# Kernel tuning notes

Hardware: AMD Instinct MI355X
Metric: run time of the kernel (lower is better)

Reference implementation:

```python
import jax, jax.numpy as jnp
import numpy as np

B, C, H, NP, M = 32, 768, 12, 196, 64
D = C // H
GRID = 14  # sqrt(196)
NG = 1 + NP  # cls + patches = 197
EPS = 1e-5


def _ln(x, w, b):
    mu = x.mean(-1, keepdims=True)
    var = ((x - mu) ** 2).mean(-1, keepdims=True)
    return (x - mu) * jax.lax.rsqrt(var + EPS) * w + b


def setup_inputs() -> dict:
    key = jax.random.key(0)
    ks = jax.random.split(key, 14)
    std = 0.02
    return {
        "x": jax.random.normal(ks[0], (B, NG + M, C), dtype=jnp.float32),
        "ps": jax.random.uniform(ks[1], (B, M, 2), dtype=jnp.float32) * 224.0,
        "ns": jax.random.randint(ks[2], (B,), 1, M + 1, dtype=jnp.int32),
        "norm1_w": jnp.ones((C,), jnp.float32),
        "norm1_b": jnp.zeros((C,), jnp.float32),
        "qkv_w": jax.random.normal(ks[3], (3 * C, C), jnp.float32) * std,
        "proj_w": jax.random.normal(ks[4], (C, C), jnp.float32) * std,
        "proj_b": jnp.zeros((C,), jnp.float32),
        "norm2_w": jnp.ones((C,), jnp.float32),
        "norm2_b": jnp.zeros((C,), jnp.float32),
        "fc1_w": jax.random.normal(ks[5], (4 * C, C), jnp.float32) * std,
        "fc1_b": jnp.zeros((4 * C,), jnp.float32),
        "fc2_w": jax.random.normal(ks[6], (C, 4 * C), jnp.float32) * std,
        "fc2_b": jnp.zeros((C,), jnp.float32),
    }


def reference(x, ps, ns, norm1_w, norm1_b, qkv_w, proj_w, proj_b,
              norm2_w, norm2_b, fc1_w, fc1_b, fc2_w, fc2_b):
    Bn, Nt, Cd = x.shape  # Nt = 1 + 196 + M
    scale = D ** -0.5

    h = _ln(x, norm1_w, norm1_b)
    qkv = (h @ qkv_w.T).reshape(Bn, Nt, 3, H, D).transpose(2, 0, 3, 1, 4)  # [3,B,H,Nt,D]
    q, k, v = qkv[0], qkv[1], qkv[2]

    # ---- global attention over cls + patch tokens (first 197) ----
    attn = jnp.einsum('bhnd,bhmd->bhnm', q[:, :, :NG], k[:, :, :NG]) * scale
    attn = jax.nn.softmax(attn, axis=-1)
    xg = jnp.einsum('bhnm,bhmd->bhnd', attn, v[:, :, :NG])
    xg = xg.transpose(0, 2, 1, 3).reshape(Bn, NG, Cd)  # [B,197,C]

    # ---- keypoint bilinear-gather attention (get_single_filter_matrix) ----
    pos = ps / 16.0  # [B,M,2]; pos[...,1] -> row (dim 4), pos[...,0] -> col (dim 5)
    c0 = jnp.clip(jnp.floor(pos[..., 0]), 0, GRID - 1).astype(jnp.int32)
    c1 = jnp.clip(jnp.ceil(pos[..., 0]), 0, GRID - 1).astype(jnp.int32)
    r0 = jnp.clip(jnp.floor(pos[..., 1]), 0, GRID - 1).astype(jnp.int32)
    r1 = jnp.clip(jnp.ceil(pos[..., 1]), 0, GRID - 1).astype(jnp.int32)
    # neighbor order: top_left, top_right, bottom_left, bottom_right
    rows = jnp.stack([r0, r1, r0, r1], axis=-1)  # [B,M,4]
    cols = jnp.stack([c0, c0, c1, c1], axis=-1)
    flat = rows * GRID + cols  # [B,M,4] flat index into 196 patch tokens

    kp = k[:, :, 1:NG]  # [B,H,196,D]
    vp = v[:, :, 1:NG]
    idx = jnp.broadcast_to(flat.reshape(Bn, 1, M * 4, 1), (Bn, H, M * 4, D))
    knb = jnp.take_along_axis(kp, idx, axis=2).reshape(Bn, H, M, 4, D)
    vnb = jnp.take_along_axis(vp, idx, axis=2).reshape(Bn, H, M, 4, D)

    qk = q[:, :, NG:]  # keypoint queries [B,H,M,D]
    a = jnp.einsum('bhmd,bhmjd->bhmj', qk, knb)  # no scale, per original
    a = jax.nn.softmax(a, axis=-1)
    kout = jnp.einsum('bhmj,bhmjd->bhmd', a, vnb)
    kout = kout.transpose(0, 2, 1, 3).reshape(Bn, M, Cd)

    y = jnp.concatenate([xg, kout], axis=1) @ proj_w.T + proj_b
    x = x + y

    h2 = _ln(x, norm2_w, norm2_b)
    h2 = jax.nn.gelu(h2 @ fc1_w.T + fc1_b, approximate=False)
    x = x + (h2 @ fc2_w.T + fc2_b)
    return x
```

## Files before the change

### kernel.cpp

```cpp
#include <hip/hip_runtime.h>

typedef unsigned short u16;
typedef unsigned int u32;
typedef u16 u16x8 __attribute__((ext_vector_type(8)));
typedef u16 u16x4 __attribute__((ext_vector_type(4)));
typedef float f32x4 __attribute__((ext_vector_type(4)));
typedef __bf16 bf16x8 __attribute__((ext_vector_type(8)));

#define NHEAD 12
#define NT 261
#define NGL 197
#define CDIM 768
#define KT 14
#define PS_STRIDE 232
#define VT_STRIDE 232

__device__ __forceinline__ float bf2f(u16 u) {
    u32 x = ((u32)u) << 16;
    float f;
    __builtin_memcpy(&f, &x, 4);
    return f;
}
__device__ __forceinline__ u16 f2bf(float f) {
    u32 x;
    __builtin_memcpy(&x, &f, 4);
    x = (x + 0x7fffu + ((x >> 16) & 1u)) >> 16;
    return (u16)x;
}

#define GLD_LDS16(g, l) \
    __builtin_amdgcn_global_load_lds((const __attribute__((address_space(1))) void*)(g), \
                                     (__attribute__((address_space(3))) void*)(l), 16, 0, 0)
#define WAITV(n) asm volatile("s_waitcnt vmcnt(" #n ")" ::: "memory")
#define BARM() asm volatile("s_barrier" ::: "memory")

struct CvArgs {
    const float* in[4];
    u16* out[4];
    int n4[4];
};
__global__ __launch_bounds__(256) void convk4(CvArgs a) {
    int y = blockIdx.y;
    const float* in = a.in[y];
    u16* out = a.out[y];
    int n4 = a.n4[y];
    int i = blockIdx.x * 256 + threadIdx.x;
    if (i >= n4) return;
    float4 v = ((const float4*)in)[i];
    u16x4 o;
    o[0] = f2bf(v.x); o[1] = f2bf(v.y); o[2] = f2bf(v.z); o[3] = f2bf(v.w);
    ((u16x4*)out)[i] = o;
}

__global__ __launch_bounds__(256) void ln_k(const float* __restrict__ in, const float* __restrict__ w,
                                            const float* __restrict__ bia, u16* __restrict__ out) {
    int row = blockIdx.x;
    int tid = threadIdx.x;
    const float* r = in + (size_t)row * CDIM;
    float v0 = r[tid], v1 = r[tid + 256], v2 = r[tid + 512];
    float s = v0 + v1 + v2;
    float ss = v0 * v0 + v1 * v1 + v2 * v2;
#pragma unroll
    for (int off = 32; off; off >>= 1) {
        s += __shfl_xor(s, off);
        ss += __shfl_xor(ss, off);
    }
    __shared__ float ls[4], lss[4];
    int wv = tid >> 6;
    if ((tid & 63) == 0) { ls[wv] = s; lss[wv] = ss; }
    __syncthreads();
    s = ls[0] + ls[1] + ls[2] + ls[3];
    ss = lss[0] + lss[1] + lss[2] + lss[3];
    float mu = s * (1.f / 768.f);
    float var = ss * (1.f / 768.f) - mu * mu;
    float inv = rsqrtf(var + 1e-5f);
    u16* o = out + (size_t)row * CDIM;
    o[tid]       = f2bf((v0 - mu) * inv * w[tid]       + bia[tid]);
    o[tid + 256] = f2bf((v1 - mu) * inv * w[tid + 256] + bia[tid + 256]);
    o[tid + 512] = f2bf((v2 - mu) * inv * w[tid + 512] + bia[tid + 512]);
}

template <int EPI>
__global__ __launch_bounds__(512, 2) void gemm5(const u16* __restrict__ A, const u16* __restrict__ Bw,
                                                int M, int N, int K, int nbn,
                                                const float* __restrict__ bias,
                                                void* __restrict__ outp) {
    __shared__ __align__(16) u16 sm[2][32768];
    const int tid = threadIdx.x;
    const int nwg = gridDim.x;
    const int q = nwg >> 3, r = nwg & 7;
    const int xcd = blockIdx.x & 7, within = blockIdx.x >> 3;
    const int id2 = (xcd < r ? xcd * (q + 1) : r * (q + 1) + (xcd - r) * q) + within;
    const int bm = id2 / nbn, bn = id2 % nbn;
    const int lane = tid & 63, wv = tid >> 6;
    const int wr = wv >> 2, wc = wv & 3;
    const int l15 = lane & 15, lg = lane >> 4;
    const int arow0 = bm * 256, brow0 = bn * 256;
    const int nt = K >> 6;

    const int srow = tid >> 3;
    const int sk = ((tid & 7) ^ (srow & 7)) * 8;
    const u16* gA[4];
    const u16* gB[4];
#pragma unroll
    for (int i = 0; i < 4; ++i) {
        int ar = arow0 + i * 64 + srow;
        if (ar >= M) ar = M - 1;
        gA[i] = A + (size_t)ar * K + sk;
        gB[i] = Bw + (size_t)(brow0 + i * 64 + srow) * K + sk;
    }

    auto STAGE = [&](int tt) {
        u16* sb = sm[tt & 1];
        const size_t ko = (size_t)tt * 64;
#pragma unroll
        for (int i = 0; i < 4; ++i) GLD_LDS16(gA[i] + ko, sb + i * 4096 + tid * 8);
#pragma unroll
        for (int i = 0; i < 4; ++i) GLD_LDS16(gB[i] + ko, sb + 16384 + i * 4096 + tid * 8);
    };

    f32x4 acc[8][4] = {};
    const int xb = l15 & 7;

    STAGE(0);
    for (int t = 0; t < nt; ++t) {
        if (t + 1 < nt) {
            STAGE(t + 1);
            WAITV(8);
        } else {
            WAITV(0);
        }
        BARM();
        const u16* sb = sm[t & 1];
        bf16x8 bq[4][2];
#pragma unroll
        for (int ni = 0; ni < 4; ++ni)
#pragma unroll
            for (int kk = 0; kk < 2; ++kk)
                bq[ni][kk] = *(const bf16x8*)(sb + 16384 + (wc * 64 + ni * 16 + l15) * 64 + (((kk << 2) | lg) ^ xb) * 8);
#pragma unroll
        for (int mi = 0; mi < 8; ++mi) {
            const u16* arow = sb + (wr * 128 + mi * 16 + l15) * 64;
            bf16x8 a0 = *(const bf16x8*)(arow + ((lg ^ xb) * 8));
            bf16x8 a1 = *(const bf16x8*)(arow + (((4 | lg) ^ xb) * 8));
#pragma unroll
            for (int ni = 0; ni < 4; ++ni) {
                acc[mi][ni] = __builtin_amdgcn_mfma_f32_16x16x32_bf16(a0, bq[ni][0], acc[mi][ni], 0, 0, 0);
                acc[mi][ni] = __builtin_amdgcn_mfma_f32_16x16x32_bf16(a1, bq[ni][1], acc[mi][ni], 0, 0, 0);
            }
        }
        if (t + 2 < nt) BARM();
    }

#pragma unroll
    for (int mi = 0; mi < 8; ++mi) {
        int row0 = arow0 + wr * 128 + mi * 16 + lg * 4;
#pragma unroll
        for (int ni = 0; ni < 4; ++ni) {
            int col = brow0 + wc * 64 + ni * 16 + l15;
            float bb = (EPI == 0) ? 0.f : bias[col];
#pragma unroll
            for (int rr = 0; rr < 4; ++rr) {
                int row = row0 + rr;
                if (row < M) {
                    float v = acc[mi][ni][rr] + bb;
                    if (EPI == 2) {
                        float z = v + 0.044715f * v * v * v;
                        v = v / (1.f + __expf(-1.5957691216f * z));
                    }
                    ((u16*)outp)[(size_t)row * N + col] = f2bf(v);
                }
            }
        }
    }
}

template <int EPI>
__global__ __launch_bounds__(256, 2) void gemm4n(const u16* __restrict__ A, const u16* __restrict__ Bw,
                                                 int M, int N, int K, int nbn,
                                                 const float* __restrict__ bias,
                                                 const float* __restrict__ resid, void* __restrict__ outp) {
    constexpr int SLOT = 128 * 64 + 8192;
    __shared__ __align__(16) u16 sm[2 * SLOT];
    const int tid = threadIdx.x;
    const int nwg = gridDim.x;
    const int q = nwg >> 3, r = nwg & 7;
    const int xcd = blockIdx.x & 7, within = blockIdx.x >> 3;
    const int id2 = (xcd < r ? xcd * (q + 1) : r * (q + 1) + (xcd - r) * q) + within;
    const int bm = id2 / nbn, bn = id2 % nbn;
    const int lane = tid & 63, wv = tid >> 6;
    const int wr = wv >> 1, wc = wv & 1;
    const int l15 = lane & 15, lg = lane >> 4;
    const int arow0 = bm * 128, brow0 = bn * 128;
    const int nt = K >> 6;

    const int srow = tid >> 3;
    const int sk = ((tid & 7) ^ (srow & 7)) * 8;
    const u16* gA[4];
    const u16* gB[4];
#pragma unroll
    for (int i = 0; i < 4; ++i) {
        int ar = arow0 + i * 32 + srow;
        if (ar >= M) ar = M - 1;
        gA[i] = A + (size_t)ar * K + sk;
        gB[i] = Bw + (size_t)(brow0 + i * 32 + srow) * K + sk;
    }

    auto STAGE = [&](int tt) {
        u16* sb = sm + (tt & 1) * SLOT;
        const size_t ko = (size_t)tt * 64;
#pragma unroll
        for (int i = 0; i < 4; ++i) GLD_LDS16(gA[i] + ko, sb + i * 2048 + tid * 8);
#pragma unroll
        for (int i = 0; i < 4; ++i) GLD_LDS16(gB[i] + ko, sb + 8192 + i * 2048 + tid * 8);
    };

    f32x4 acc[4][4] = {};
    const int xb = l15 & 7;

    STAGE(0);
    for (int t = 0; t < nt; ++t) {
        if (t + 1 < nt) {
            STAGE(t + 1);
            WAITV(8);
        } else {
            WAITV(0);
        }
        BARM();
        const u16* sb = sm + (t & 1) * SLOT;
        bf16x8 af[4][2], bq[4][2];
#pragma unroll
        for (int mi = 0; mi < 4; ++mi)
#pragma unroll
            for (int kk = 0; kk < 2; ++kk)
                af[mi][kk] = *(const bf16x8*)(sb + (wr * 64 + mi * 16 + l15) * 64 + (((kk << 2) | lg) ^ xb) * 8);
#pragma unroll
        for (int ni = 0; ni < 4; ++ni)
#pragma unroll
            for (int kk = 0; kk < 2; ++kk)
                bq[ni][kk] = *(const bf16x8*)(sb + 8192 + (wc * 64 + ni * 16 + l15) * 64 + (((kk << 2) | lg) ^ xb) * 8);
#pragma unroll
        for (int mi = 0; mi < 4; ++mi)
#pragma unroll
            for (int ni = 0; ni < 4; ++ni) {
                acc[mi][ni] = __builtin_amdgcn_mfma_f32_16x16x32_bf16(af[mi][0], bq[ni][0], acc[mi][ni], 0, 0, 0);
                acc[mi][ni] = __builtin_amdgcn_mfma_f32_16x16x32_bf16(af[mi][1], bq[ni][1], acc[mi][ni], 0, 0, 0);
            }
        if (t + 2 < nt) BARM();
    }

#pragma unroll
    for (int mi = 0; mi < 4; ++mi) {
        int row0 = arow0 + wr * 64 + mi * 16 + lg * 4;
#pragma unroll
        for (int ni = 0; ni < 4; ++ni) {
            int col = brow0 + wc * 64 + ni * 16 + l15;
            float bb = bias[col];
#pragma unroll
            for (int rr = 0; rr < 4; ++rr) {
                int row = row0 + rr;
                if (row < M) {
                    float v = acc[mi][ni][rr] + bb + resid[(size_t)row * N + col];
                    ((float*)outp)[(size_t)row * N + col] = v;
                }
            }
        }
    }
}

__global__ __launch_bounds__(256) void attn_global_mfma(const u16* __restrict__ qkv, u16* __restrict__ Z) {
    __shared__ __align__(16) u16 lds0[4 * 16 * PS_STRIDE];
    __shared__ __align__(16) u16 Vt[64 * VT_STRIDE];
    const int tid = threadIdx.x;
    const int blk = blockIdx.x;
    const int qt = blk & 3;
    const int bh = blk >> 2;
    const int h = bh % NHEAD, b = bh / NHEAD;
    const int lane = tid & 63, wv = tid >> 6;
    const int l15 = lane & 15, lg = lane >> 4;
    const u16* base = qkv + (size_t)b * NT * 2304;

    for (int c = tid; c < 224 * 8; c += 256) {
        int row = c >> 3, ch = c & 7;
        u16x8 v = {};
        if (row < NGL) v = *(const u16x8*)(base + (size_t)row * 2304 + 768 + h * 64 + ch * 8);
        int byte = row * 128 + ((ch * 16) ^ ((row & 7) << 4));
        *(u16x8*)((char*)lds0 + byte) = v;
    }
    for (int c = tid; c < 112 * 8; c += 256) {
        int mp = c >> 3, dch = c & 7;
        int m0 = mp * 2;
        u16x8 a0 = {}, a1 = {};
        if (m0 < NGL)     a0 = *(const u16x8*)(base + (size_t)m0 * 2304 + 1536 + h * 64 + dch * 8);
        if (m0 + 1 < NGL) a1 = *(const u16x8*)(base + (size_t)(m0 + 1) * 2304 + 1536 + h * 64 + dch * 8);
#pragma unroll
        for (int j = 0; j < 8; ++j) {
            u32 pk = (u32)a0[j] | ((u32)a1[j] << 16);
            *(u32*)((char*)Vt + (size_t)(dch * 8 + j) * (VT_STRIDE * 2) + m0 * 2) = pk;
        }
    }
    const int q0 = qt * 64 + wv * 16;
    int qrow = q0 + l15; if (qrow > NGL - 1) qrow = NGL - 1;
    bf16x8 aq0 = *(const bf16x8*)(base + (size_t)qrow * 2304 + h * 64 + lg * 8);
    bf16x8 aq1 = *(const bf16x8*)(base + (size_t)qrow * 2304 + h * 64 + 32 + lg * 8);
    __syncthreads();

    f32x4 s[KT];
    const int sw = (l15 & 7) << 4;
#pragma unroll
    for (int t = 0; t < KT; ++t) {
        const char* krow = (const char*)lds0 + (t * 16 + l15) * 128;
        bf16x8 bk0 = *(const bf16x8*)(krow + ((lg * 16) ^ sw));
        bf16x8 bk1 = *(const bf16x8*)(krow + ((64 + lg * 16) ^ sw));
        f32x4 acc = {};
        acc = __builtin_amdgcn_mfma_f32_16x16x32_bf16(aq0, bk0, acc, 0, 0, 0);
        acc = __builtin_amdgcn_mfma_f32_16x16x32_bf16(aq1, bk1, acc, 0, 0, 0);
        s[t] = acc * 0.125f;
    }
    float mx[4] = {-1e30f, -1e30f, -1e30f, -1e30f};
#pragma unroll
    for (int t = 0; t < KT; ++t)
#pragma unroll
        for (int r = 0; r < 4; ++r) mx[r] = fmaxf(mx[r], s[t][r]);
#pragma unroll
    for (int off = 1; off < 16; off <<= 1)
#pragma unroll
        for (int r = 0; r < 4; ++r) mx[r] = fmaxf(mx[r], __shfl_xor(mx[r], off));
    float sum[4] = {};
#pragma unroll
    for (int t = 0; t < KT; ++t) {
        bool valid = (t * 16 + l15) < NGL;
#pragma unroll
        for (int r = 0; r < 4; ++r) {
            float e = valid ? __expf(s[t][r] - mx[r]) : 0.f;
            s[t][r] = e;
            sum[r] += e;
        }
    }
#pragma unroll
    for (int off = 1; off < 16; off <<= 1)
#pragma unroll
        for (int r = 0; r < 4; ++r) sum[r] += __shfl_xor(sum[r], off);
    float inv[4];
#pragma unroll
    for (int r = 0; r < 4; ++r) inv[r] = 1.f / sum[r];

    __syncthreads();
    u16* Pw = lds0 + wv * 16 * PS_STRIDE;
#pragma unroll
    for (int t = 0; t < KT; ++t)
#pragma unroll
        for (int r = 0; r < 4; ++r)
            Pw[(4 * lg + r) * PS_STRIDE + t * 16 + l15] = f2bf(s[t][r] * inv[r]);

    f32x4 o[4] = {};
#pragma unroll
    for (int ks = 0; ks < 7; ++ks) {
        bf16x8 pa = *(const bf16x8*)(Pw + l15 * PS_STRIDE + ks * 32 + lg * 8);
#pragma unroll
        for (int dt = 0; dt < 4; ++dt) {
            bf16x8 bv = *(const bf16x8*)((const char*)Vt + (size_t)(dt * 16 + l15) * (VT_STRIDE * 2) + ks * 64 + lg * 16);
            o[dt] = __builtin_amdgcn_mfma_f32_16x16x32_bf16(pa, bv, o[dt], 0, 0, 0);
        }
    }
#pragma unroll
    for (int dt = 0; dt < 4; ++dt)
#pragma unroll
        for (int r = 0; r < 4; ++r) {
            int q = q0 + 4 * lg + r;
            if (q < NGL) Z[((size_t)b * NT + q) * CDIM + h * 64 + dt * 16 + l15] = f2bf(o[dt][r]);
        }
}

__global__ __launch_bounds__(64) void attn_neigh(const u16* __restrict__ qkv, const float* __restrict__ ps,
                                                 u16* __restrict__ Z) {
    int blk = blockIdx.x;
    int b = blk >> 6, m = blk & 63;
    int lane = threadIdx.x;
    float px = ps[((size_t)b * 64 + m) * 2 + 0] * (1.f / 16.f);
    float py = ps[((size_t)b * 64 + m) * 2 + 1] * (1.f / 16.f);
    int c0 = min(max((int)floorf(px), 0), 13);
    int c1 = min(max((int)ceilf(px), 0), 13);
    int r0 = min(max((int)floorf(py), 0), 13);
    int r1 = min(max((int)ceilf(py), 0), 13);
    int tok[4];
    tok[0] = 1 + r0 * 14 + c0;
    tok[1] = 1 + r1 * 14 + c0;
    tok[2] = 1 + r0 * 14 + c1;
    tok[3] = 1 + r1 * 14 + c1;
    const size_t rowq = ((size_t)b * NT + NGL + m) * 2304;
#pragma unroll 1
    for (int h = 0; h < NHEAD; ++h) {
        float qv = bf2f(qkv[rowq + h * 64 + lane]);
        float a[4];
#pragma unroll
        for (int j = 0; j < 4; ++j) {
            float p = qv * bf2f(qkv[((size_t)b * NT + tok[j]) * 2304 + 768 + h * 64 + lane]);
#pragma unroll
            for (int off = 32; off; off >>= 1) p += __shfl_xor(p, off);
            a[j] = p;
        }
        float mx = fmaxf(fmaxf(a[0], a[1]), fmaxf(a[2], a[3]));
        float e0 = expf(a[0] - mx), e1 = expf(a[1] - mx), e2 = expf(a[2] - mx), e3 = expf(a[3] - mx);
        float inv = 1.f / (e0 + e1 + e2 + e3);
        float v0 = bf2f(qkv[((size_t)b * NT + tok[0]) * 2304 + 1536 + h * 64 + lane]);
        float v1 = bf2f(qkv[((size_t)b * NT + tok[1]) * 2304 + 1536 + h * 64 + lane]);
        float v2 = bf2f(qkv[((size_t)b * NT + tok[2]) * 2304 + 1536 + h * 64 + lane]);
        float v3 = bf2f(qkv[((size_t)b * NT + tok[3]) * 2304 + 1536 + h * 64 + lane]);
        float o = (e0 * v0 + e1 * v1 + e2 * v2 + e3 * v3) * inv;
        Z[((size_t)b * NT + NGL + m) * CDIM + h * 64 + lane] = f2bf(o);
    }
}

extern "C" void kernel_launch(void* const* d_in, const int* in_sizes, int n_in,
                              void* d_out, int out_size, void* d_ws, size_t ws_size,
                              hipStream_t stream) {
    const float* x      = (const float*)d_in[0];
    const float* ps     = (const float*)d_in[1];
    const float* n1w    = (const float*)d_in[3];
    const float* n1b    = (const float*)d_in[4];
    const float* qkv_w  = (const float*)d_in[5];
    const float* proj_w = (const float*)d_in[6];
    const float* proj_b = (const float*)d_in[7];
    const float* n2w    = (const float*)d_in[8];
    const float* n2b    = (const float*)d_in[9];
    const float* fc1_w  = (const float*)d_in[10];
    const float* fc1_b  = (const float*)d_in[11];
    const float* fc2_w  = (const float*)d_in[12];
    const float* fc2_b  = (const float*)d_in[13];

    char* ws = (char*)d_ws;
    const int M = 32 * NT;
    u16* hbuf  = (u16*)ws;
    u16* qkvb  = (u16*)(ws + 12828672);
    u16* Zb    = (u16*)(ws + 12828672 + 38486016);
    u16* Gb    = (u16*)(ws + 12828672);
    float* x1  = (float*)(ws + 64143360);
    u16* wq    = (u16*)(ws + 89800704);
    u16* wp    = wq + 2304 * 768;
    u16* w1    = wp + 768 * 768;
    u16* w2    = w1 + 3072 * 768;

    CvArgs cv;
    cv.in[0] = qkv_w;  cv.out[0] = wq; cv.n4[0] = 2304 * 768 / 4;
    cv.in[1] = proj_w; cv.out[1] = wp; cv.n4[1] = 768 * 768 / 4;
    cv.in[2] = fc1_w;  cv.out[2] = w1; cv.n4[2] = 3072 * 768 / 4;
    cv.in[3] = fc2_w;  cv.out[3] = w2; cv.n4[3] = 768 * 3072 / 4;
    convk4<<<dim3((3072 * 768 / 4 + 255) / 256, 4), 256, 0, stream>>>(cv);

    ln_k<<<M, 256, 0, stream>>>(x, n1w, n1b, hbuf);
    gemm5<0><<<33 * 9, 512, 0, stream>>>(hbuf, wq, M, 2304, 768, 9, nullptr, qkvb);
    attn_global_mfma<<<32 * NHEAD * 4, 256, 0, stream>>>(qkvb, Zb);
    attn_neigh<<<32 * 64, 64, 0, stream>>>(qkvb, ps, Zb);
    gemm4n<1><<<66 * 6, 256, 0, stream>>>(Zb, wp, M, 768, 768, 6, proj_b, x, x1);
    ln_k<<<M, 256, 0, stream>>>(x1, n2w, n2b, hbuf);
    gemm5<2><<<33 * 12, 512, 0, stream>>>(hbuf, w1, M, 3072, 768, 12, fc1_b, Gb);
    gemm4n<1><<<66 * 6, 256, 0, stream>>>(Gb, w2, M, 768, 3072, 6, fc2_b, x1, (float*)d_out);
}
```

Baseline: 308.7 us.

## Fuse weight conversion with LN1, merge neighbor attention into global attention launch

Combines the fp32→bf16 weight conversion and the first LayerNorm into one launch, and folds the keypoint neighbor-attention into extra blocks of the global attention kernel. LayerNorm is rewritten to use one wavefront per row with float4 loads and no LDS reduction. The aim is fewer kernel launches and less per-launch and barrier overhead. Larger fused grids may mix heterogeneous block work.

Result: faster. 302.0 us (-2.2%).

```diff
diff --git a/kernel.cpp b/kernel.cpp
--- a/kernel.cpp
+++ b/kernel.cpp
@@ -39,45 +39,71 @@
     u16* out[4];
     int n4[4];
 };
-__global__ __launch_bounds__(256) void convk4(CvArgs a) {
-    int y = blockIdx.y;
-    const float* in = a.in[y];
-    u16* out = a.out[y];
-    int n4 = a.n4[y];
-    int i = blockIdx.x * 256 + threadIdx.x;
-    if (i >= n4) return;
-    float4 v = ((const float4*)in)[i];
-    u16x4 o;
-    o[0] = f2bf(v.x); o[1] = f2bf(v.y); o[2] = f2bf(v.z); o[3] = f2bf(v.w);
-    ((u16x4*)out)[i] = o;
-}
-
-__global__ __launch_bounds__(256) void ln_k(const float* __restrict__ in, const float* __restrict__ w,
-                                            const float* __restrict__ bia, u16* __restrict__ out) {
-    int row = blockIdx.x;
-    int tid = threadIdx.x;
-    const float* r = in + (size_t)row * CDIM;
-    float v0 = r[tid], v1 = r[tid + 256], v2 = r[tid + 512];
-    float s = v0 + v1 + v2;
-    float ss = v0 * v0 + v1 * v1 + v2 * v2;
+
+__device__ __forceinline__ void ln_row(const float* __restrict__ in, const float* __restrict__ w,
+                                       const float* __restrict__ bia, u16* __restrict__ out,
+                                       int row, int lane) {
+    const float4* r = (const float4*)(in + (size_t)row * CDIM);
+    float4 a = r[lane], b4 = r[lane + 64], c4 = r[lane + 128];
+    float s  = a.x + a.y + a.z + a.w + b4.x + b4.y + b4.z + b4.w + c4.x + c4.y + c4.z + c4.w;
+    float ss = a.x*a.x + a.y*a.y + a.z*a.z + a.w*a.w
+             + b4.x*b4.x + b4.y*b4.y + b4.z*b4.z + b4.w*b4.w
+             + c4.x*c4.x + c4.y*c4.y + c4.z*c4.z + c4.w*c4.w;
 #pragma unroll
     for (int off = 32; off; off >>= 1) {
-        s += __shfl_xor(s, off);
+        s  += __shfl_xor(s, off);
         ss += __shfl_xor(ss, off);
     }
-    __shared__ float ls[4], lss[4];
-    int wv = tid >> 6;
-    if ((tid & 63) == 0) { ls[wv] = s; lss[wv] = ss; }
-    __syncthreads();
-    s = ls[0] + ls[1] + ls[2] + ls[3];
-    ss = lss[0] + lss[1] + lss[2] + lss[3];
     float mu = s * (1.f / 768.f);
     float var = ss * (1.f / 768.f) - mu * mu;
     float inv = rsqrtf(var + 1e-5f);
+    const float4* wp = (const float4*)w;
+    const float4* bp = (const float4*)bia;
     u16* o = out + (size_t)row * CDIM;
-    o[tid]       = f2bf((v0 - mu) * inv * w[tid]       + bia[tid]);
-    o[tid + 256] = f2bf((v1 - mu) * inv * w[tid + 256] + bia[tid + 256]);
-    o[tid + 512] = f2bf((v2 - mu) * inv * w[tid + 512] + bia[tid + 512]);
+#pragma unroll
+    for (int t = 0; t < 3; ++t) {
+        float4 v = (t == 0) ? a : (t == 1) ? b4 : c4;
+        float4 ww = wp[lane + t * 64], bb = bp[lane + t * 64];
+        u16x4 ov;
+        ov[0] = f2bf((v.x - mu) * inv * ww.x + bb.x);
+        ov[1] = f2bf((v.y - mu) * inv * ww.y + bb.y);
+        ov[2] = f2bf((v.z - mu) * inv * ww.z + bb.z);
+        ov[3] = f2bf((v.w - mu) * inv * ww.w + bb.w);
+        *(u16x4*)(o + t * 256 + lane * 4) = ov;
+    }
+}
+
+__global__ __launch_bounds__(256) void pre_k(const float* __restrict__ x, const float* __restrict__ w,
+                                             const float* __restrict__ bia, u16* __restrict__ out,
+                                             int nrows, CvArgs cv) {
+    if (blockIdx.y == 0) {
+        int i = blockIdx.x * 256 + threadIdx.x;
+        int s0 = cv.n4[0], s1 = s0 + cv.n4[1], s2 = s1 + cv.n4[2], s3 = s2 + cv.n4[3];
+        const float* in;
+        u16* o;
+        int base;
+        if (i < s0)      { in = cv.in[0]; o = cv.out[0]; base = 0; }
+        else if (i < s1) { in = cv.in[1]; o = cv.out[1]; base = s0; }
+        else if (i < s2) { in = cv.in[2]; o = cv.out[2]; base = s1; }
+        else if (i < s3) { in = cv.in[3]; o = cv.out[3]; base = s2; }
+        else return;
+        int j = i - base;
+        float4 v = ((const float4*)in)[j];
+        u16x4 ov;
+        ov[0] = f2bf(v.x); ov[1] = f2bf(v.y); ov[2] = f2bf(v.z); ov[3] = f2bf(v.w);
+        ((u16x4*)o)[j] = ov;
+    } else {
+        int lane = threadIdx.x & 63, wv = threadIdx.x >> 6;
+        int row = blockIdx.x * 4 + wv;
+        if (row < nrows) ln_row(x, w, bia, out, row, lane);
+    }
+}
+
+__global__ __launch_bounds__(256) void ln_w(const float* __restrict__ in, const float* __restrict__ w,
+                                            const float* __restrict__ bia, u16* __restrict__ out, int nrows) {
+    int lane = threadIdx.x & 63, wv = threadIdx.x >> 6;
+    int row = blockIdx.x * 4 + wv;
+    if (row < nrows) ln_row(in, w, bia, out, row, lane);
 }
 
 template <int EPI>
@@ -175,7 +201,6 @@
     }
 }
 
-template <int EPI>
 __global__ __launch_bounds__(256, 2) void gemm4n(const u16* __restrict__ A, const u16* __restrict__ Bw,
                                                  int M, int N, int K, int nbn,
                                                  const float* __restrict__ bias,
@@ -268,15 +293,57 @@
     }
 }
 
-__global__ __launch_bounds__(256) void attn_global_mfma(const u16* __restrict__ qkv, u16* __restrict__ Z) {
+__global__ __launch_bounds__(256) void attn_fused(const u16* __restrict__ qkv, const float* __restrict__ ps,
+                                                  u16* __restrict__ Z) {
     __shared__ __align__(16) u16 lds0[4 * 16 * PS_STRIDE];
     __shared__ __align__(16) u16 Vt[64 * VT_STRIDE];
     const int tid = threadIdx.x;
+    const int lane = tid & 63, wv = tid >> 6;
+
+    if (blockIdx.x >= 1536) {
+        int idx = blockIdx.x - 1536;
+        int b = idx >> 4;
+        int m = (idx & 15) * 4 + wv;
+        float px = ps[((size_t)b * 64 + m) * 2 + 0] * (1.f / 16.f);
+        float py = ps[((size_t)b * 64 + m) * 2 + 1] * (1.f / 16.f);
+        int c0 = min(max((int)floorf(px), 0), 13);
+        int c1 = min(max((int)ceilf(px), 0), 13);
+        int r0 = min(max((int)floorf(py), 0), 13);
+        int r1 = min(max((int)ceilf(py), 0), 13);
+        int tok[4];
+        tok[0] = 1 + r0 * 14 + c0;
+        tok[1] = 1 + r1 * 14 + c0;
+        tok[2] = 1 + r0 * 14 + c1;
+        tok[3] = 1 + r1 * 14 + c1;
+        const size_t rowq = ((size_t)b * NT + NGL + m) * 2304;
+#pragma unroll 1
+        for (int h = 0; h < NHEAD; ++h) {
+            float qv = bf2f(qkv[rowq + h * 64 + lane]);
+            float a[4];
+#pragma unroll
+            for (int j = 0; j < 4; ++j) {
+                float p = qv * bf2f(qkv[((size_t)b * NT + tok[j]) * 2304 + 768 + h * 64 + lane]);
+#pragma unroll
+                for (int off = 32; off; off >>= 1) p += __shfl_xor(p, off);
+                a[j] = p;
+            }
+            float mx = fmaxf(fmaxf(a[0], a[1]), fmaxf(a[2], a[3]));
+            float e0 = expf(a[0] - mx), e1 = expf(a[1] - mx), e2 = expf(a[2] - mx), e3 = expf(a[3] - mx);
+            float inv = 1.f / (e0 + e1 + e2 + e3);
+            float v0 = bf2f(qkv[((size_t)b * NT + tok[0]) * 2304 + 1536 + h * 64 + lane]);
+            float v1 = bf2f(qkv[((size_t)b * NT + tok[1]) * 2304 + 1536 + h * 64 + lane]);
+            float v2 = bf2f(qkv[((size_t)b * NT + tok[2]) * 2304 + 1536 + h * 64 + lane]);
+            float v3 = bf2f(qkv[((size_t)b * NT + tok[3]) * 2304 + 1536 + h * 64 + lane]);
+            float o = (e0 * v0 + e1 * v1 + e2 * v2 + e3 * v3) * inv;
+            Z[((size_t)b * NT + NGL + m) * CDIM + h * 64 + lane] = f2bf(o);
+        }
+        return;
+    }
+
     const int blk = blockIdx.x;
     const int qt = blk & 3;
     const int bh = blk >> 2;
     const int h = bh % NHEAD, b = bh / NHEAD;
-    const int lane = tid & 63, wv = tid >> 6;
     const int l15 = lane & 15, lg = lane >> 4;
     const u16* base = qkv + (size_t)b * NT * 2304;
 
@@ -370,46 +437,6 @@
             int q = q0 + 4 * lg + r;
             if (q < NGL) Z[((size_t)b * NT + q) * CDIM + h * 64 + dt * 16 + l15] = f2bf(o[dt][r]);
         }
-}
-
-__global__ __launch_bounds__(64) void attn_neigh(const u16* __restrict__ qkv, const float* __restrict__ ps,
-                                                 u16* __restrict__ Z) {
-    int blk = blockIdx.x;
-    int b = blk >> 6, m = blk & 63;
-    int lane = threadIdx.x;
-    float px = ps[((size_t)b * 64 + m) * 2 + 0] * (1.f / 16.f);
-    float py = ps[((size_t)b * 64 + m) * 2 + 1] * (1.f / 16.f);
-    int c0 = min(max((int)floorf(px), 0), 13);
-    int c1 = min(max((int)ceilf(px), 0), 13);
-    int r0 = min(max((int)floorf(py), 0), 13);
-    int r1 = min(max((int)ceilf(py), 0), 13);
-    int tok[4];
-    tok[0] = 1 + r0 * 14 + c0;
-    tok[1] = 1 + r1 * 14 + c0;
-    tok[2] = 1 + r0 * 14 + c1;
-    tok[3] = 1 + r1 * 14 + c1;
-    const size_t rowq = ((size_t)b * NT + NGL + m) * 2304;
-#pragma unroll 1
-    for (int h = 0; h < NHEAD; ++h) {
-        float qv = bf2f(qkv[rowq + h * 64 + lane]);
-        float a[4];
-#pragma unroll
-        for (int j = 0; j < 4; ++j) {
-            float p = qv * bf2f(qkv[((size_t)b * NT + tok[j]) * 2304 + 768 + h * 64 + lane]);
-#pragma unroll
-            for (int off = 32; off; off >>= 1) p += __shfl_xor(p, off);
-            a[j] = p;
-        }
-        float mx = fmaxf(fmaxf(a[0], a[1]), fmaxf(a[2], a[3]));
-        float e0 = expf(a[0] - mx), e1 = expf(a[1] - mx), e2 = expf(a[2] - mx), e3 = expf(a[3] - mx);
-        float inv = 1.f / (e0 + e1 + e2 + e3);
-        float v0 = bf2f(qkv[((size_t)b * NT + tok[0]) * 2304 + 1536 + h * 64 + lane]);
-        float v1 = bf2f(qkv[((size_t)b * NT + tok[1]) * 2304 + 1536 + h * 64 + lane]);
-        float v2 = bf2f(qkv[((size_t)b * NT + tok[2]) * 2304 + 1536 + h * 64 + lane]);
-        float v3 = bf2f(qkv[((size_t)b * NT + tok[3]) * 2304 + 1536 + h * 64 + lane]);
-        float o = (e0 * v0 + e1 * v1 + e2 * v2 + e3 * v3) * inv;
-        Z[((size_t)b * NT + NGL + m) * CDIM + h * 64 + lane] = f2bf(o);
-    }
 }
 
 extern "C" void kernel_launch(void* const* d_in, const int* in_sizes, int n_in,
@@ -446,14 +473,12 @@
     cv.in[1] = proj_w; cv.out[1] = wp; cv.n4[1] = 768 * 768 / 4;
     cv.in[2] = fc1_w;  cv.out[2] = w1; cv.n4[2] = 3072 * 768 / 4;
     cv.in[3] = fc2_w;  cv.out[3] = w2; cv.n4[3] = 768 * 3072 / 4;
-    convk4<<<dim3((3072 * 768 / 4 + 255) / 256, 4), 256, 0, stream>>>(cv);
-
-    ln_k<<<M, 256, 0, stream>>>(x, n1w, n1b, hbuf);
+
+    pre_k<<<dim3(6912, 2), 256, 0, stream>>>(x, n1w, n1b, hbuf, M, cv);
     gemm5<0><<<33 * 9, 512, 0, stream>>>(hbuf, wq, M, 2304, 768, 9, nullptr, qkvb);
-    attn_global_mfma<<<32 * NHEAD * 4, 256, 0, stream>>>(qkvb, Zb);
-    attn_neigh<<<32 * 64, 64, 0, stream>>>(qkvb, ps, Zb);
-    gemm4n<1><<<66 * 6, 256, 0, stream>>>(Zb, wp, M, 768, 768, 6, proj_b, x, x1);
-    ln_k<<<M, 256, 0, stream>>>(x1, n2w, n2b, hbuf);
+    attn_fused<<<2048, 256, 0, stream>>>(qkvb, ps, Zb);
+    gemm4n<<<66 * 6, 256, 0, stream>>>(Zb, wp, M, 768, 768, 6, proj_b, x, x1);
+    ln_w<<<2088, 256, 0, stream>>>(x1, n2w, n2b, hbuf, M);
     gemm5<2><<<33 * 12, 512, 0, stream>>>(hbuf, w1, M, 3072, 768, 12, fc1_b, Gb);
-    gemm4n<1><<<66 * 6, 256, 0, stream>>>(Gb, w2, M, 768, 3072, 6, fc2_b, x1, (float*)d_out);
-}
+    gemm4n<<<66 * 6, 256, 0, stream>>>(Gb, w2, M, 768, 3072, 6, fc2_b, x1, (float*)d_out);
+}
```
